# Performance work log

Hardware: AMD Instinct MI355X
Metric: run time of the kernel (lower is better)

Reference implementation:

```python
import jax, jax.numpy as jnp
import numpy as np

H, DH = 16, 64  # heads, dim_head (inner_dim = 1024)


def _sdpa(q, k, v):
    # q: (B, Q, D), k/v: (B, K, D); scale = 1/sqrt(D) as in F.scaled_dot_product_attention
    scale = 1.0 / jnp.sqrt(jnp.asarray(q.shape[-1], q.dtype))
    s = jnp.einsum('bqd,bkd->bqk', q, k) * scale
    return jnp.einsum('bqk,bkd->bqd', jax.nn.softmax(s, axis=-1), v)


def setup_inputs() -> dict:
    key = jax.random.key(0)
    ks = jax.random.split(key, 3)
    b, f, n, dim = 8, 16, 196, 1024
    N = 1 + f * n  # CLS + frames*patches = 3137
    x = jax.random.normal(ks[0], (b, N, dim), jnp.float32)
    w_qkv = jax.random.normal(ks[1], (3 * H * DH, dim), jnp.float32) * 0.02
    w_out = jax.random.normal(ks[2], (dim, H * DH), jnp.float32) * 0.02
    b_out = jnp.zeros((dim,), jnp.float32)
    return {"x": x, "w_qkv": w_qkv, "w_out": w_out, "b_out": b_out, "f": f}


def reference(x, w_qkv, w_out, b_out, f):
    b, N, dim = x.shape
    n = (N - 1) // f  # patches per frame

    qkv = x @ w_qkv.T  # (b, N, 3*H*DH)
    q, k, v = jnp.split(qkv, 3, axis=-1)

    def to_bh(t):  # 'b n (h d) -> (b h) n d'
        return t.reshape(b, N, H, DH).transpose(0, 2, 1, 3).reshape(b * H, N, DH)

    q, k, v = map(to_bh, (q, k, v))

    cls_q, q_ = q[:, :1], q[:, 1:]
    cls_k, k_ = k[:, :1], k[:, 1:]
    cls_v, v_ = v[:, :1], v[:, 1:]

    # CLS token attends over all tokens
    cls_out = _sdpa(cls_q, k, v)  # (b*H, 1, DH)

    # spatial attention: '(b h) (f n) d -> (b h f) n d'
    def to_space(t):
        return t.reshape(b * H, f, n, DH).reshape(b * H * f, n, DH)

    q_, k_, v_ = map(to_space, (q_, k_, v_))

    # repeat_interleave CLS k/v over the f groups, then prepend
    ck = jnp.repeat(cls_k, f, axis=0)  # (b*H*f, 1, DH)
    cv = jnp.repeat(cls_v, f, axis=0)
    k_ = jnp.concatenate((ck, k_), axis=1)  # (b*H*f, n+1, DH)
    v_ = jnp.concatenate((cv, v_), axis=1)

    out = _sdpa(q_, k_, v_)  # (b*H*f, n, DH)
    out = out.reshape(b * H, f * n, DH)  # '(b f) n d -> b (f n) d'
    out = jnp.concatenate((cls_out, out), axis=1)  # (b*H, N, DH)
    # '(b h) n d -> b n (h d)'
    out = out.reshape(b, H, N, DH).transpose(0, 2, 1, 3).reshape(b, N, H * DH)
    return out @ w_out.T + b_out
```

## Files before the change

kernel.cpp:

```cpp
#include <hip/hip_runtime.h>
#include <cstdint>
#include <cstddef>

#define DEVINL __device__ __forceinline__

typedef __attribute__((ext_vector_type(8))) short short8;
typedef __attribute__((ext_vector_type(4))) float f32x4;
typedef unsigned short u16;
typedef unsigned int u32;

DEVINL u16 f2b(float f) {
    u32 u = __float_as_uint(f);
    u32 r = (u + 0x7fffu + ((u >> 16) & 1u)) >> 16;
    return (u16)r;
}
DEVINL float b2f(u16 h) { return __uint_as_float(((u32)h) << 16); }

DEVINL void gl_lds16(const void* g, void* l) {
    __builtin_amdgcn_global_load_lds(
        (const __attribute__((address_space(1))) void*)g,
        (__attribute__((address_space(3))) void*)l, 16, 0, 0);
}

#define MROWS   25096
#define NTOK    3137
#define QE      25698304
#define LOG2E   1.4426950408889634f
#define SCL2    0.1803368801111204f

__global__ __launch_bounds__(256) void cvt_kernel(const float* __restrict__ in,
                                                  u16* __restrict__ out, int n4) {
    int i = blockIdx.x * blockDim.x + threadIdx.x;
    int stride = gridDim.x * blockDim.x;
    for (int j = i; j < n4; j += stride) {
        float4 v = ((const float4*)in)[j];
        ushort4 o;
        o.x = f2b(v.x); o.y = f2b(v.y); o.z = f2b(v.z); o.w = f2b(v.w);
        ((ushort4*)out)[j] = o;
    }
}

#define LDS_BUF 32768
#define NTILES  16

template <int MODE>
__global__ __launch_bounds__(512, 2) void gemm256(const u16* __restrict__ A,
                                                  const u16* __restrict__ B,
                                                  u16* __restrict__ q_out,
                                                  u16* __restrict__ k_out,
                                                  u16* __restrict__ v_out,
                                                  const float* __restrict__ bias,
                                                  float* __restrict__ f_out, int M) {
    __shared__ u16 lds[2 * LDS_BUF];
    const int tid = threadIdx.x, lane = tid & 63, w = tid >> 6;
    const int Mm1 = M - 1;

    const u32 nwg = gridDim.x * gridDim.y;
    const u32 orig = blockIdx.y * gridDim.x + blockIdx.x;
    const u32 q8 = nwg >> 3, r8 = nwg & 7, xcd = orig & 7, rest = orig >> 3;
    const u32 wg = (xcd < r8 ? xcd * (q8 + 1) : r8 * (q8 + 1) + (xcd - r8) * q8) + rest;
    const int m0 = (int)(wg / gridDim.x) * 256;
    const int n0 = (int)(wg % gridDim.x) * 256;

    const int wm = w >> 2, wn = w & 3;

    const int stRow = lane >> 2;
    const int stCol = (((lane & 3) ^ ((lane >> 3) & 3)) << 3);

    const int slotOff = (((lane >> 4) ^ ((lane >> 1) & 3)) << 3);
    const int rdA = (wm * 128 + (lane & 15)) * 32 + slotOff;
    const int rdB = (wn * 64 + (lane & 15)) * 32 + slotOff + 16384;

#define STAGE_A(NB, KK, KT) do {                                              \
    _Pragma("unroll") for (int j_ = 0; j_ < 2; ++j_) {                        \
        const int c_ = (w << 1) | j_;                                         \
        int r_ = m0 + c_ * 16 + stRow; if (r_ > Mm1) r_ = Mm1;                \
        gl_lds16(A + (size_t)r_ * 1024 + (KT) + (KK) * 32 + stCol,            \
                 lds + (NB) + (KK) * 8192 + c_ * 512);                        \
    } } while (0)

#define STAGE_B(NB, KK, KT) do {                                              \
    _Pragma("unroll") for (int j_ = 0; j_ < 2; ++j_) {                        \
        const int c_ = (w << 1) | j_;                                         \
        const int r_ = n0 + c_ * 16 + stRow;                                  \
        gl_lds16(B + (size_t)r_ * 1024 + (KT) + (KK) * 32 + stCol,            \
                 lds + (NB) + 16384 + (KK) * 8192 + c_ * 512);                \
    } } while (0)

#define LDA4(CB, KK, MB) do {                                                 \
    _Pragma("unroll") for (int i_ = 0; i_ < 4; ++i_)                          \
        aF[i_] = *(const short8*)&lds[(CB) + (KK) * 8192 + rdA +              \
                                      ((MB) + i_) * 16 * 32];                 \
    } while (0)

#define LDB4(CB, KK) do {                                                     \
    _Pragma("unroll") for (int i_ = 0; i_ < 4; ++i_)                          \
        bF[i_] = *(const short8*)&lds[(CB) + (KK) * 8192 + rdB +              \
                                      i_ * 16 * 32];                          \
    } while (0)

#define MFMA16(MB) do {                                                       \
    _Pragma("unroll") for (int i_ = 0; i_ < 4; ++i_)                          \
        _Pragma("unroll") for (int n_ = 0; n_ < 4; ++n_)                      \
            acc[(MB) + i_][n_] = __builtin_amdgcn_mfma_f32_16x16x32_bf16(     \
                aF[i_], bF[n_], acc[(MB) + i_][n_], 0, 0, 0);                 \
    } while (0)

#define LGKM0_FENCE() do {                                                    \
    asm volatile("s_waitcnt lgkmcnt(0)" ::: "memory");                        \
    __builtin_amdgcn_sched_barrier(0); } while (0)

    f32x4 acc[8][4];
    const f32x4 zf = {0.f, 0.f, 0.f, 0.f};
#pragma unroll
    for (int i = 0; i < 8; ++i)
#pragma unroll
        for (int j = 0; j < 4; ++j) acc[i][j] = zf;

    STAGE_A(0, 0, 0);
    STAGE_B(0, 0, 0);
    STAGE_A(0, 1, 0);
    STAGE_B(0, 1, 0);
    asm volatile("s_waitcnt vmcnt(4)" ::: "memory");
    __builtin_amdgcn_sched_barrier(0);
    __builtin_amdgcn_s_barrier();

    for (int T = 0; T < NTILES; ++T) {
        const int cb = (T & 1) * LDS_BUF;
        const int nb = ((T + 1) & 1) * LDS_BUF;
        const bool pf = (T < NTILES - 1);
        const int kt1 = (T + 1) * 64;

        short8 aF[4], bF[4];

        LDA4(cb, 0, 0);
        LDB4(cb, 0);
        if (pf) STAGE_A(nb, 0, kt1);
        __builtin_amdgcn_s_barrier();
        LGKM0_FENCE();
        __builtin_amdgcn_s_setprio(1);
        MFMA16(0);
        __builtin_amdgcn_s_setprio(0);
        __builtin_amdgcn_s_barrier();

        LDA4(cb, 0, 4);
        if (pf) STAGE_B(nb, 0, kt1);
        __builtin_amdgcn_s_barrier();
        LGKM0_FENCE();
        __builtin_amdgcn_s_setprio(1);
        MFMA16(4);
        __builtin_amdgcn_s_setprio(0);
        if (pf) { asm volatile("s_waitcnt vmcnt(4)" ::: "memory"); }
        else    { asm volatile("s_waitcnt vmcnt(0)" ::: "memory"); }
        __builtin_amdgcn_sched_barrier(0);
        __builtin_amdgcn_s_barrier();

        LDA4(cb, 1, 0);
        LDB4(cb, 1);
        if (pf) STAGE_A(nb, 1, kt1);
        __builtin_amdgcn_s_barrier();
        LGKM0_FENCE();
        __builtin_amdgcn_s_setprio(1);
        MFMA16(0);
        __builtin_amdgcn_s_setprio(0);
        __builtin_amdgcn_s_barrier();

        LDA4(cb, 1, 4);
        if (pf) STAGE_B(nb, 1, kt1);
        __builtin_amdgcn_s_barrier();
        LGKM0_FENCE();
        __builtin_amdgcn_s_setprio(1);
        MFMA16(4);
        __builtin_amdgcn_s_setprio(0);
        if (pf) {
            asm volatile("s_waitcnt vmcnt(4)" ::: "memory");
            __builtin_amdgcn_sched_barrier(0);
        }
        __builtin_amdgcn_s_barrier();
    }

#pragma unroll
    for (int m = 0; m < 8; ++m) {
#pragma unroll
        for (int n = 0; n < 4; ++n) {
#pragma unroll
            for (int r = 0; r < 4; ++r) {
                const int gm = m0 + wm * 128 + m * 16 + ((lane >> 4) << 2) + r;
                if (gm < M) {
                    const int gc = n0 + wn * 64 + n * 16 + (lane & 15);
                    if (MODE == 0) {
                        const int t = gc >> 10;
                        const int h = (gc >> 6) & 15;
                        const int d = gc & 63;
                        const u32 bb = (u32)gm / 3137u;
                        const u32 nn = (u32)gm - bb * 3137u;
                        u16* dst = (t == 0) ? q_out : (t == 1) ? k_out : v_out;
                        dst[(((size_t)(bb * 16 + h)) * NTOK + nn) * 64 + d] =
                            f2b(acc[m][n][r]);
                    } else {
                        f_out[(size_t)gm * 1024 + gc] = acc[m][n][r] + bias[gc];
                    }
                }
            }
        }
    }
#undef STAGE_A
#undef STAGE_B
#undef LDA4
#undef LDB4
#undef MFMA16
#undef LGKM0_FENCE
}

#define CSZ 393
__global__ __launch_bounds__(256) void attn_cls_part(const u16* __restrict__ qb,
                                                     const u16* __restrict__ kb,
                                                     const u16* __restrict__ vb,
                                                     float* __restrict__ part) {
    const int bid = blockIdx.x;
    const int bh = bid >> 3, c = bid & 7;
    const size_t base = (size_t)bh * NTOK * 64;
    const int tid = threadIdx.x, lane = tid & 63, wid = tid >> 6;
    const int j0 = c * CSZ;
    const int cnt = min(NTOK - j0, CSZ);

    __shared__ float qs[64];
    __shared__ float sc[CSZ];
    __shared__ float redbuf[8];
    __shared__ float ored[4][64];

    if (tid < 64) qs[tid] = b2f(qb[base + tid]);
    __syncthreads();

    for (int j = tid; j < cnt; j += 256) {
        const u16* kr = kb + base + (size_t)(j0 + j) * 64;
        float acc = 0.f;
#pragma unroll
        for (int c2 = 0; c2 < 8; ++c2) {
            short8 v8 = *(const short8*)(kr + c2 * 8);
#pragma unroll
            for (int t = 0; t < 8; ++t) acc += qs[c2 * 8 + t] * b2f((u16)v8[t]);
        }
        sc[j] = acc * 0.125f;
    }
    __syncthreads();

    float mx = -1e30f;
    for (int j = tid; j < cnt; j += 256) mx = fmaxf(mx, sc[j]);
#pragma unroll
    for (int m = 32; m >= 1; m >>= 1) mx = fmaxf(mx, __shfl_xor(mx, m));
    if (lane == 0) redbuf[wid] = mx;
    __syncthreads();
    mx = fmaxf(fmaxf(redbuf[0], redbuf[1]), fmaxf(redbuf[2], redbuf[3]));

    float sum = 0.f;
    for (int j = tid; j < cnt; j += 256) {
        float p = exp2f((sc[j] - mx) * LOG2E);
        sc[j] = p;
        sum += p;
    }
#pragma unroll
    for (int m = 32; m >= 1; m >>= 1) sum += __shfl_xor(sum, m);
    if (lane == 0) redbuf[4 + wid] = sum;
    __syncthreads();
    const float tot = redbuf[4] + redbuf[5] + redbuf[6] + redbuf[7];

    const int d = tid & 63, g = tid >> 6;
    float o = 0.f;
    for (int j = g; j < cnt; j += 4)
        o += sc[j] * b2f(vb[base + (size_t)(j0 + j) * 64 + d]);
    ored[g][d] = o;
    __syncthreads();

    float* pb = part + (size_t)bid * 66;
    if (tid < 64) pb[2 + tid] = ored[0][tid] + ored[1][tid] + ored[2][tid] + ored[3][tid];
    else if (tid == 64) pb[0] = mx;
    else if (tid == 65) pb[1] = tot;
}

__global__ __launch_bounds__(64) void attn_cls_fin(const float* __restrict__ part,
                                                   u16* __restrict__ attnb) {
    const int bh = blockIdx.x, d = threadIdx.x;
    const int bb = bh >> 4, h = bh & 15;
    float m = -1e30f;
#pragma unroll
    for (int c = 0; c < 8; ++c) m = fmaxf(m, part[(size_t)(bh * 8 + c) * 66]);
    float t = 0.f, o = 0.f;
#pragma unroll
    for (int c = 0; c < 8; ++c) {
        const float* pb = part + (size_t)(bh * 8 + c) * 66;
        const float w = exp2f((pb[0] - m) * LOG2E);
        t += w * pb[1];
        o += w * pb[2 + d];
    }
    attnb[(size_t)bb * NTOK * 1024 + h * 64 + d] = f2b(o / t);
}

__global__ __launch_bounds__(256, 3) void attn_spatial(const u16* __restrict__ qb,
                                                       const u16* __restrict__ kb,
                                                       const u16* __restrict__ vb,
                                                       u16* __restrict__ attnb) {
    const int blk = blockIdx.x;
    const int bh = blk >> 4, fi = blk & 15;
    const int bb = bh >> 4, h = bh & 15;
    const int tid = threadIdx.x, lane = tid & 63, wid = tid >> 6;
    const int hi = lane >> 4, lo = lane & 15;
    const size_t kvbase = (size_t)bh * NTOK * 64;

    __shared__ u16 Kl[208 * 64];
    __shared__ u16 Vt[64 * 208];

    const short8 z8 = {0, 0, 0, 0, 0, 0, 0, 0};

    for (int idx = tid; idx < 208 * 8; idx += 256) {
        const int j = idx >> 3, c = idx & 7;
        short8 kval = z8;
        if (j < 197) {
            const int n = (j == 0) ? 0 : (1 + fi * 196 + (j - 1));
            kval = *(const short8*)(kb + kvbase + (size_t)n * 64 + c * 8);
            const short8 v8 = *(const short8*)(vb + kvbase + (size_t)n * 64 + c * 8);
#pragma unroll
            for (int t0 = 0; t0 < 8; ++t0) {
                const int t = (t0 + c) & 7;
                Vt[(c * 8 + t) * 208 + j] = (u16)v8[t];
            }
        } else {
#pragma unroll
            for (int t = 0; t < 8; ++t) Vt[(c * 8 + t) * 208 + j] = 0;
        }
        *(short8*)(Kl + ((j * 64 + c * 8) ^ ((j & 7) << 3))) = kval;
    }
    __syncthreads();

    const int ksw = (lo & 7) << 3;
    const int src0 = lo + ((hi & 1) << 5);
    const int src1 = src0 + 16;
    const f32x4 zf = {0.f, 0.f, 0.f, 0.f};

    for (int mf = wid; mf < 13; mf += 4) {
        int qr = mf * 16 + lo; if (qr > 195) qr = 195;
        const u16* qp = qb + kvbase + (size_t)(1 + fi * 196 + qr) * 64 + hi * 8;
        const short8 qb0 = *(const short8*)(qp);
        const short8 qb1 = *(const short8*)(qp + 32);

        f32x4 s[13];
#pragma unroll
        for (int nf = 0; nf < 13; ++nf) s[nf] = zf;
#pragma unroll
        for (int nf = 0; nf < 13; ++nf) {
            const int e0 = (nf * 16 + lo) * 64 + hi * 8;
            const short8 a0 = *(const short8*)(Kl + (e0 ^ ksw));
            const short8 a1 = *(const short8*)(Kl + ((e0 + 32) ^ ksw));
            s[nf] = __builtin_amdgcn_mfma_f32_16x16x32_bf16(a0, qb0, s[nf], 0, 0, 0);
            s[nf] = __builtin_amdgcn_mfma_f32_16x16x32_bf16(a1, qb1, s[nf], 0, 0, 0);
        }

        float mx = s[0][0];
#pragma unroll
        for (int nf = 0; nf < 13; ++nf)
#pragma unroll
            for (int reg = 0; reg < 4; ++reg) mx = fmaxf(mx, s[nf][reg]);
        mx = fmaxf(mx, __shfl_xor(mx, 16));
        mx = fmaxf(mx, __shfl_xor(mx, 32));
        const float mC = mx * SCL2;
        float sum = 0.f;
#pragma unroll
        for (int nf = 0; nf < 13; ++nf)
#pragma unroll
            for (int reg = 0; reg < 4; ++reg) {
                const float p = exp2f(fmaf(s[nf][reg], SCL2, -mC));
                s[nf][reg] = p;
                sum += p;
            }
        sum += __shfl_xor(sum, 16);
        sum += __shfl_xor(sum, 32);
        const float rls = 1.0f / (sum - 11.0f * exp2f(-mC));

        u32 w0[13], w1[13];
#pragma unroll
        for (int nf = 0; nf < 13; ++nf) {
            const float p0 = s[nf][0] * rls, p1 = s[nf][1] * rls;
            const float p2 = s[nf][2] * rls, p3 = s[nf][3] * rls;
            asm("v_cvt_pk_bf16_f32 %0, %1, %2" : "=v"(w0[nf]) : "v"(p0), "v"(p1));
            asm("v_cvt_pk_bf16_f32 %0, %1, %2" : "=v"(w1[nf]) : "v"(p2), "v"(p3));
        }

        f32x4 o[4];
#pragma unroll
        for (int i = 0; i < 4; ++i) o[i] = zf;
#pragma unroll
        for (int kk = 0; kk < 7; ++kk) {
            u32 x0, x1, x2, x3;
            if (kk < 6) {
                const u32 aA0 = __shfl(w0[2 * kk], src0), aA1 = __shfl(w1[2 * kk], src0);
                const u32 aA2 = __shfl(w0[2 * kk], src1), aA3 = __shfl(w1[2 * kk], src1);
                const u32 aB0 = __shfl(w0[2 * kk + 1], src0), aB1 = __shfl(w1[2 * kk + 1], src0);
                const u32 aB2 = __shfl(w0[2 * kk + 1], src1), aB3 = __shfl(w1[2 * kk + 1], src1);
                const bool lh = hi < 2;
                x0 = lh ? aA0 : aB0; x1 = lh ? aA1 : aB1;
                x2 = lh ? aA2 : aB2; x3 = lh ? aA3 : aB3;
            } else {
                const u32 aA0 = __shfl(w0[12], src0), aA1 = __shfl(w1[12], src0);
                const u32 aA2 = __shfl(w0[12], src1), aA3 = __shfl(w1[12], src1);
                const bool lh = hi < 2;
                x0 = lh ? aA0 : 0u; x1 = lh ? aA1 : 0u;
                x2 = lh ? aA2 : 0u; x3 = lh ? aA3 : 0u;
            }
            union { u32 u[4]; short8 v; } pu;
            pu.u[0] = x0; pu.u[1] = x1; pu.u[2] = x2; pu.u[3] = x3;
            const short8 pa = pu.v;
#pragma unroll
            for (int nf2 = 0; nf2 < 4; ++nf2) {
                short8 bv = z8;
                if (kk < 6 || hi < 2)
                    bv = *(const short8*)(Vt + (nf2 * 16 + lo) * 208 + kk * 32 + hi * 8);
                o[nf2] = __builtin_amdgcn_mfma_f32_16x16x32_bf16(pa, bv, o[nf2], 0, 0, 0);
            }
        }

#pragma unroll
        for (int nf2 = 0; nf2 < 4; ++nf2)
#pragma unroll
            for (int reg = 0; reg < 4; ++reg) {
                const int r = mf * 16 + hi * 4 + reg;
                if (r < 196) {
                    const int d = nf2 * 16 + lo;
                    const size_t nn = 1 + fi * 196 + r;
                    attnb[((size_t)bb * NTOK + nn) * 1024 + h * 64 + d] =
                        f2b(o[nf2][reg]);
                }
            }
    }
}

extern "C" void kernel_launch(void* const* d_in, const int* in_sizes, int n_in,
                              void* d_out, int out_size, void* d_ws, size_t ws_size,
                              hipStream_t stream) {
    const float* x = (const float*)d_in[0];
    const float* w_qkv = (const float*)d_in[1];
    const float* w_out = (const float*)d_in[2];
    const float* b_out = (const float*)d_in[3];

    const size_t need = ((size_t)QE * 2 + 3145728 + 1048576) * 2;
    if (ws_size < need) {
        hipMemsetAsync(d_out, 0, (size_t)out_size * 4, stream);
        return;
    }

    u16* vb = (u16*)d_ws;
    u16* xab = vb + QE;
    u16* wqb = xab + QE;
    u16* wob = wqb + 3145728;
    u16* qb = (u16*)d_out;
    u16* kb = qb + QE;
    float* outf = (float*)d_out;
    float* clsp = (float*)wqb;

    cvt_kernel<<<2048, 256, 0, stream>>>(x, xab, QE / 4);
    cvt_kernel<<<2048, 256, 0, stream>>>(w_qkv, wqb, 3145728 / 4);
    cvt_kernel<<<1024, 256, 0, stream>>>(w_out, wob, 1048576 / 4);

    gemm256<0><<<dim3(12, 99), 512, 0, stream>>>(xab, wqb, qb, kb, vb, nullptr,
                                                 nullptr, MROWS);
    attn_cls_part<<<1024, 256, 0, stream>>>(qb, kb, vb, clsp);
    attn_cls_fin<<<128, 64, 0, stream>>>(clsp, xab);
    attn_spatial<<<2048, 256, 0, stream>>>(qb, kb, vb, xab);
    gemm256<1><<<dim3(4, 99), 512, 0, stream>>>(xab, wob, nullptr, nullptr, nullptr,
                                                b_out, outf, MROWS);
}
```

Measured before the change: 457.2 us.

## Restructure GEMM inner loop to prefetch LDS fragments ahead of MFMAs

Reworks the bf16 GEMM main loop so LDS fragment reads for the next MFMA phase are issued before the current MFMA block, using separate register sets per sub-phase. It drops the explicit lgkmcnt(0) waits and halves the number of s_barriers per phase, letting LDS reads overlap with MFMA execution. The cost is higher VGPR pressure from the extra fragment arrays, which could hurt the 2-waves-per-SIMD occupancy. It also reorders the global-to-LDS staging and vmcnt waits, which risks races if the compiler-inserted waits are not enough.

```diff
diff --git a/kernel.cpp b/kernel.cpp
--- a/kernel.cpp
+++ b/kernel.cpp
@@ -39,6 +39,7 @@
         ((ushort4*)out)[j] = o;
     }
 }
+
 
 #define LDS_BUF 32768
 #define NTILES  16
@@ -87,27 +88,27 @@
                  lds + (NB) + 16384 + (KK) * 8192 + c_ * 512);                \
     } } while (0)
 
-#define LDA4(CB, KK, MB) do {                                                 \
+#define LDA4(DST, CB, KK, MB) do {                                            \
     _Pragma("unroll") for (int i_ = 0; i_ < 4; ++i_)                          \
-        aF[i_] = *(const short8*)&lds[(CB) + (KK) * 8192 + rdA +              \
-                                      ((MB) + i_) * 16 * 32];                 \
+        DST[i_] = *(const short8*)&lds[(CB) + (KK) * 8192 + rdA +             \
+                                       ((MB) + i_) * 16 * 32];                \
     } while (0)
 
-#define LDB4(CB, KK) do {                                                     \
+#define LDB4(DST, CB, KK) do {                                                \
     _Pragma("unroll") for (int i_ = 0; i_ < 4; ++i_)                          \
-        bF[i_] = *(const short8*)&lds[(CB) + (KK) * 8192 + rdB +              \
-                                      i_ * 16 * 32];                          \
+        DST[i_] = *(const short8*)&lds[(CB) + (KK) * 8192 + rdB +             \
+                                       i_ * 16 * 32];                         \
     } while (0)
 
-#define MFMA16(MB) do {                                                       \
+#define MFMA16(AV, BV, MB) do {                                               \
     _Pragma("unroll") for (int i_ = 0; i_ < 4; ++i_)                          \
         _Pragma("unroll") for (int n_ = 0; n_ < 4; ++n_)                      \
             acc[(MB) + i_][n_] = __builtin_amdgcn_mfma_f32_16x16x32_bf16(     \
-                aF[i_], bF[n_], acc[(MB) + i_][n_], 0, 0, 0);                 \
+                AV[i_], BV[n_], acc[(MB) + i_][n_], 0, 0, 0);                 \
     } while (0)
 
-#define LGKM0_FENCE() do {                                                    \
-    asm volatile("s_waitcnt lgkmcnt(0)" ::: "memory");                        \
+#define PHASE_BAR() do {                                                      \
+    __builtin_amdgcn_s_barrier();                                             \
     __builtin_amdgcn_sched_barrier(0); } while (0)
 
     f32x4 acc[8][4];
@@ -123,7 +124,7 @@
     STAGE_B(0, 1, 0);
     asm volatile("s_waitcnt vmcnt(4)" ::: "memory");
     __builtin_amdgcn_sched_barrier(0);
-    __builtin_amdgcn_s_barrier();
+    PHASE_BAR();
 
     for (int T = 0; T < NTILES; ++T) {
         const int cb = (T & 1) * LDS_BUF;
@@ -131,52 +132,44 @@
         const bool pf = (T < NTILES - 1);
         const int kt1 = (T + 1) * 64;
 
-        short8 aF[4], bF[4];
-
-        LDA4(cb, 0, 0);
-        LDB4(cb, 0);
+        short8 a0m0[4], a0m4[4], a1m0[4], a1m4[4], b0[4], b1[4];
+
+        LDA4(a0m0, cb, 0, 0);
+        LDB4(b0,   cb, 0);
+        LDA4(a0m4, cb, 0, 4);
         if (pf) STAGE_A(nb, 0, kt1);
-        __builtin_amdgcn_s_barrier();
-        LGKM0_FENCE();
         __builtin_amdgcn_s_setprio(1);
-        MFMA16(0);
+        MFMA16(a0m0, b0, 0);
         __builtin_amdgcn_s_setprio(0);
-        __builtin_amdgcn_s_barrier();
-
-        LDA4(cb, 0, 4);
-        if (pf) STAGE_B(nb, 0, kt1);
-        __builtin_amdgcn_s_barrier();
-        LGKM0_FENCE();
-        __builtin_amdgcn_s_setprio(1);
-        MFMA16(4);
-        __builtin_amdgcn_s_setprio(0);
-        if (pf) { asm volatile("s_waitcnt vmcnt(4)" ::: "memory"); }
+        if (pf) { asm volatile("s_waitcnt vmcnt(2)" ::: "memory"); }
         else    { asm volatile("s_waitcnt vmcnt(0)" ::: "memory"); }
         __builtin_amdgcn_sched_barrier(0);
-        __builtin_amdgcn_s_barrier();
-
-        LDA4(cb, 1, 0);
-        LDB4(cb, 1);
+        PHASE_BAR();
+
+        LDA4(a1m0, cb, 1, 0);
+        LDB4(b1,   cb, 1);
+        if (pf) STAGE_B(nb, 0, kt1);
+        __builtin_amdgcn_s_setprio(1);
+        MFMA16(a0m4, b0, 4);
+        __builtin_amdgcn_s_setprio(0);
+        PHASE_BAR();
+
+        LDA4(a1m4, cb, 1, 4);
         if (pf) STAGE_A(nb, 1, kt1);
-        __builtin_amdgcn_s_barrier();
-        LGKM0_FENCE();
         __builtin_amdgcn_s_setprio(1);
-        MFMA16(0);
+        MFMA16(a1m0, b1, 0);
         __builtin_amdgcn_s_setprio(0);
-        __builtin_amdgcn_s_barrier();
-
-        LDA4(cb, 1, 4);
+        PHASE_BAR();
+
         if (pf) STAGE_B(nb, 1, kt1);
-        __builtin_amdgcn_s_barrier();
-        LGKM0_FENCE();
         __builtin_amdgcn_s_setprio(1);
-        MFMA16(4);
+        MFMA16(a1m4, b1, 4);
         __builtin_amdgcn_s_setprio(0);
         if (pf) {
             asm volatile("s_waitcnt vmcnt(4)" ::: "memory");
             __builtin_amdgcn_sched_barrier(0);
         }
-        __builtin_amdgcn_s_barrier();
+        PHASE_BAR();
     }
 
 #pragma unroll
@@ -209,7 +202,7 @@
 #undef LDA4
 #undef LDB4
 #undef MFMA16
-#undef LGKM0_FENCE
+#undef PHASE_BAR
 }
 
 #define CSZ 393
```

After: 449.4 us. Within noise of the previous version (-1.7%).
